# Optimization experiments

Measured on AMD Instinct MI355X. Metric: run time of the kernel, lower is better.

## Reference

```python
import jax, jax.numpy as jnp
import numpy as np

N_NODES = 16384
N_EDGES = 262144
D = 300
N_GRAPHS = 64


def setup_inputs() -> dict:
    key = jax.random.key(0)
    ks = jax.random.split(key, 16)
    s = 0.05  # small init scale for numerical stability
    inp = {
        "node_feats": jax.random.normal(ks[0], (N_NODES, D), jnp.float32),
        "W_lift": jax.random.normal(ks[1], (D, D), jnp.float32) * s,
        "b_lift": jnp.zeros((D,), jnp.float32),
        "Wf1": jax.random.normal(ks[2], (D, D), jnp.float32) * s,
        "bf1": jnp.zeros((D,), jnp.float32),
        "Wo1": jax.random.normal(ks[3], (D, D), jnp.float32) * s,
        "bo1": jnp.zeros((D,), jnp.float32),
        "Wf2": jax.random.normal(ks[4], (D, D), jnp.float32) * s,
        "bf2": jnp.zeros((D,), jnp.float32),
        "Wo2": jax.random.normal(ks[5], (D, D), jnp.float32) * s,
        "bo2": jnp.zeros((D,), jnp.float32),
        "Wf3": jax.random.normal(ks[6], (D, D), jnp.float32) * s,
        "bf3": jnp.zeros((D,), jnp.float32),
        "Wo3": jax.random.normal(ks[7], (D, D), jnp.float32) * s,
        "bo3": jnp.zeros((D,), jnp.float32),
        "W_ro": jax.random.normal(ks[8], (D, 2), jnp.float32) * s,
        "b_ro": jnp.zeros((2,), jnp.float32),
        "src": jax.random.randint(ks[9], (N_EDGES,), 0, N_NODES, jnp.int32),
        "dst": jax.random.randint(ks[10], (N_EDGES,), 0, N_NODES, jnp.int32),
        "graph_ids": jnp.sort(jax.random.randint(ks[11], (N_NODES,), 0, N_GRAPHS, jnp.int32)),
    }
    return inp


def _mp_layer(h, Wf, bf, Wo, bo, src, dst):
    # message: relu Dense on gathered src feats; reduce: segment-sum into dst nodes
    msg = jax.nn.relu(h[src] @ Wf + bf)                      # [E, D]
    agg = jax.ops.segment_sum(msg, dst, num_segments=N_NODES)  # [N, D]
    return jax.nn.relu(agg @ Wo + bo)                        # output Dense+ReLU


def reference(node_feats, W_lift, b_lift, Wf1, bf1, Wo1, bo1, Wf2, bf2, Wo2, bo2,
              Wf3, bf3, Wo3, bo3, W_ro, b_ro, src, dst, graph_ids):
    h = node_feats @ W_lift + b_lift  # lift, no activation
    h = _mp_layer(h, Wf1, bf1, Wo1, bo1, src, dst)
    h = _mp_layer(h, Wf2, bf2, Wo2, bo2, src, dst)
    h = _mp_layer(h, Wf3, bf3, Wo3, bo3, src, dst)
    probs = jax.nn.softmax(h @ W_ro + b_ro, axis=-1)         # readout Dense(softmax)
    logits = jax.ops.segment_sum(probs, graph_ids, num_segments=N_GRAPHS)  # dgl.sum_nodes
    return logits
```

## Files before the change

### kernel.cpp

```cpp
#include <hip/hip_runtime.h>
#include <hip/hip_bf16.h>

#define N_NODES 16384
#define N_EDGES 262144
#define GD 300
#define DP 320
#define N_GRAPHS 64
#define NTILE 5
#define CAP 96

typedef short bf16x8 __attribute__((ext_vector_type(8)));
typedef float f32x4 __attribute__((ext_vector_type(4)));

__device__ static inline unsigned short f2bf(float v) {
  __hip_bfloat16 b = __float2bfloat16(v);
  return __builtin_bit_cast(unsigned short, b);
}
__device__ static inline float bf2f(unsigned short u) {
  return __bfloat162float(__builtin_bit_cast(__hip_bfloat16, u));
}

#define GLOAD_LDS16(g, l)                                                    \
  __builtin_amdgcn_global_load_lds(                                          \
      (const __attribute__((address_space(1))) void*)(g),                    \
      (__attribute__((address_space(3))) void*)(l), 16, 0, 0)

constexpr int ATILE = 8192;
constexpr int AFULL = 5 * ATILE;
constexpr int BBUF = 40960;
constexpr int EPITCH = 328;
constexpr size_t WSZ = (size_t)DP * DP;
static_assert(64 * EPITCH * 2 <= AFULL + 2 * BBUF, "epilogue bounce fits");

template <bool RELU1, bool TILED, bool FUSE2, bool RO, bool CONVF>
__global__ __launch_bounds__(512, 2) void gemm_f(
    const unsigned short* __restrict__ A, const float* __restrict__ nf,
    const unsigned short* __restrict__ Wt1,
    const float* __restrict__ bias1, const unsigned short* __restrict__ Wt2,
    const float* __restrict__ bias2, unsigned short* __restrict__ C,
    const float* __restrict__ Wro, const float* __restrict__ bro,
    const int* __restrict__ gid, float* __restrict__ out) {
  __shared__ __align__(16) char smem[AFULL + 2 * BBUF];
  __shared__ float wroL[2 * DP];
  __shared__ float rowacc[2 * 64];
  __shared__ float binsL[2 * N_GRAPHS];

  const int bm = blockIdx.x * 64;
  const int t = threadIdx.x;
  const int w = t >> 6, l = t & 63;
  const int wr = w & 1;
  const int wc = w >> 1;
  const int cl = l & 15, q = l >> 4;
  const int lr = l >> 3;
  const int sg = (l & 7) ^ lr;

  if (RO) {
    for (int i = t; i < DP; i += 512) {
      wroL[2 * i] = (i < GD) ? Wro[2 * i] : 0.f;
      wroL[2 * i + 1] = (i < GD) ? Wro[2 * i + 1] : 0.f;
    }
    if (t < 128) rowacc[t] = 0.f;
    if (t < 2 * N_GRAPHS) binsL[t] = 0.f;
  }

  auto stageB = [&](const unsigned short* W, int tk, int buf) {
    char* lb = smem + AFULL + buf * BBUF;
#pragma unroll
    for (int i = 0; i < 5; ++i) {
      int c = w + 8 * i;
      GLOAD_LDS16(W + (size_t)(c * 8 + lr) * DP + tk * 64 + 8 * sg,
                  lb + c * 1024);
    }
  };

  f32x4 acc[2][5] = {};

  auto compute = [&](const char* lA, const char* lB) {
#pragma unroll
    for (int ks = 0; ks < 2; ++ks) {
      bf16x8 a[2], b[5];
#pragma unroll
      for (int m = 0; m < 2; ++m) {
        int r = wr * 32 + m * 16 + cl;
        int slot = (ks * 4 + q) ^ (r & 7);
        a[m] = *(const bf16x8*)(lA + r * 128 + slot * 16);
      }
#pragma unroll
      for (int n = 0; n < 5; ++n) {
        int r = wc * 80 + n * 16 + cl;
        int slot = (ks * 4 + q) ^ (r & 7);
        b[n] = *(const bf16x8*)(lB + r * 128 + slot * 16);
      }
#pragma unroll
      for (int m = 0; m < 2; ++m)
#pragma unroll
        for (int n = 0; n < 5; ++n)
          acc[m][n] = __builtin_amdgcn_mfma_f32_16x16x32_bf16(a[m], b[n],
                                                              acc[m][n], 0, 0, 0);
    }
  };

  stageB(Wt1, 0, 0);
  if (CONVF) {
    const int r = t >> 3;
    const int ls = t & 7;
    const float* rp = nf + (size_t)(bm + r) * GD;
#pragma unroll
    for (int p = 0; p < 5; ++p) {
      int c0 = p * 64 + ls * 8;
      bf16x8 o;
      if (c0 + 8 <= GD) {
        float4 a = *(const float4*)(rp + c0);
        float4 b = *(const float4*)(rp + c0 + 4);
        o[0] = f2bf(a.x); o[1] = f2bf(a.y); o[2] = f2bf(a.z); o[3] = f2bf(a.w);
        o[4] = f2bf(b.x); o[5] = f2bf(b.y); o[6] = f2bf(b.z); o[7] = f2bf(b.w);
      } else {
#pragma unroll
        for (int i = 0; i < 8; ++i) {
          int c = c0 + i;
          o[i] = f2bf(c < GD ? rp[c] : 0.f);
        }
      }
      *(bf16x8*)(smem + p * ATILE + r * 128 + ((ls ^ (r & 7)) << 4)) = o;
    }
    asm volatile("s_waitcnt lgkmcnt(0)" ::: "memory");
  } else {
#pragma unroll
    for (int p = 0; p < 5; ++p)
      GLOAD_LDS16(A + (size_t)(bm + w * 8 + lr) * DP + p * 64 + 8 * sg,
                  smem + p * ATILE + w * 1024);
  }

  for (int tk = 0; tk < 5; ++tk) {
    __builtin_amdgcn_s_barrier();
    if (tk + 1 < 5) {
      stageB(Wt1, tk + 1, (tk + 1) & 1);
      asm volatile("s_waitcnt vmcnt(5)" ::: "memory");
    } else if (FUSE2) {
      stageB(Wt2, 0, 1);
      asm volatile("s_waitcnt vmcnt(5)" ::: "memory");
    } else {
      asm volatile("s_waitcnt vmcnt(0)" ::: "memory");
    }
    __builtin_amdgcn_s_barrier();
    compute(smem + tk * ATILE, smem + AFULL + (tk & 1) * BBUF);
  }

  if (FUSE2) {
    __syncthreads();
#pragma unroll
    for (int n = 0; n < 5; ++n) {
      int col = wc * 80 + n * 16 + cl;
      float bv = bias1[col];
      int kt = col >> 6, kin = col & 63;
#pragma unroll
      for (int m = 0; m < 2; ++m) {
#pragma unroll
        for (int r = 0; r < 4; ++r) {
          int row = wr * 32 + m * 16 + q * 4 + r;
          float v = acc[m][n][r] + bv;
          if (RELU1) v = fmaxf(v, 0.f);
          int byte = kt * ATILE + row * 128 + (((kin >> 3) ^ (row & 7)) << 4) +
                     ((kin & 7) << 1);
          *(unsigned short*)(smem + byte) = f2bf(v);
        }
      }
    }
    asm volatile("s_waitcnt lgkmcnt(0)" ::: "memory");
#pragma unroll
    for (int m = 0; m < 2; ++m)
#pragma unroll
      for (int n = 0; n < 5; ++n) acc[m][n] = f32x4{0.f, 0.f, 0.f, 0.f};

    for (int tk = 0; tk < 5; ++tk) {
      __builtin_amdgcn_s_barrier();
      if (tk + 1 < 5) {
        stageB(Wt2, tk + 1, tk & 1);
        asm volatile("s_waitcnt vmcnt(5)" ::: "memory");
      } else {
        asm volatile("s_waitcnt vmcnt(0)" ::: "memory");
      }
      __builtin_amdgcn_s_barrier();
      compute(smem + tk * ATILE, smem + AFULL + ((tk + 1) & 1) * BBUF);
    }
  }

  if (!RO) {
    const float* bp = FUSE2 ? bias2 : bias1;
    const bool relu = FUSE2 ? true : RELU1;
    __syncthreads();
    unsigned short* ep = (unsigned short*)smem;
#pragma unroll
    for (int n = 0; n < 5; ++n) {
      int col = wc * 80 + n * 16 + cl;
      float bv = bp[col];
#pragma unroll
      for (int m = 0; m < 2; ++m) {
#pragma unroll
        for (int r = 0; r < 4; ++r) {
          int row = wr * 32 + m * 16 + q * 4 + r;
          float v = acc[m][n][r] + bv;
          if (relu) v = fmaxf(v, 0.f);
          ep[row * EPITCH + col] = f2bf(v);
        }
      }
    }
    __syncthreads();
    {
      const int row = t >> 3, c0 = (t & 7) * 40;
#pragma unroll
      for (int gch = 0; gch < 5; ++gch) {
        int col = c0 + gch * 8;
        bf16x8 v = *(const bf16x8*)(ep + row * EPITCH + col);
        size_t idx;
        if (TILED)
          idx = ((size_t)(col >> 6) * N_NODES + (bm + row)) * 64 + (col & 63);
        else
          idx = (size_t)(bm + row) * DP + col;
        *(bf16x8*)(C + idx) = v;
      }
    }
  } else {
    float bv[5];
#pragma unroll
    for (int n = 0; n < 5; ++n) bv[n] = bias1[wc * 80 + n * 16 + cl];
#pragma unroll
    for (int m = 0; m < 2; ++m) {
#pragma unroll
      for (int r = 0; r < 4; ++r) {
        float s0 = 0.f, s1 = 0.f;
#pragma unroll
        for (int n = 0; n < 5; ++n) {
          int col = wc * 80 + n * 16 + cl;
          float v = fmaxf(acc[m][n][r] + bv[n], 0.f);
          s0 += v * wroL[2 * col];
          s1 += v * wroL[2 * col + 1];
        }
#pragma unroll
        for (int off = 1; off < 16; off <<= 1) {
          s0 += __shfl_xor(s0, off);
          s1 += __shfl_xor(s1, off);
        }
        if (cl == 0) {
          int row = wr * 32 + m * 16 + q * 4 + r;
          atomicAdd(&rowacc[2 * row], s0);
          atomicAdd(&rowacc[2 * row + 1], s1);
        }
      }
    }
    __syncthreads();
    if (t < 64) {
      float d0 = rowacc[2 * t] + bro[0];
      float d1 = rowacc[2 * t + 1] + bro[1];
      float mx = fmaxf(d0, d1);
      float e0 = expf(d0 - mx), e1 = expf(d1 - mx);
      float inv = 1.f / (e0 + e1);
      int g = gid[bm + t];
      atomicAdd(&binsL[2 * g], e0 * inv);
      atomicAdd(&binsL[2 * g + 1], e1 * inv);
    }
    __syncthreads();
    if (t < 2 * N_GRAPHS) {
      float v = binsL[t];
      if (v != 0.f) atomicAdd(&out[t], v);
    }
  }
}

__global__ void scatter_pad(const int* __restrict__ src, const int* __restrict__ dst,
                            int* __restrict__ cnt, int* __restrict__ pad,
                            float* __restrict__ out, int out_n) {
  if (blockIdx.x == 0 && threadIdx.x < out_n) out[threadIdx.x] = 0.f;
  int e = blockIdx.x * blockDim.x + threadIdx.x;
  if (e >= N_EDGES) return;
  int d = dst[e];
  int pos = atomicAdd(&cnt[d], 1);
  if (pos < CAP) pad[(size_t)d * CAP + pos] = src[e];
}

__global__ __launch_bounds__(256) void spmm_tiled(
    const unsigned short* __restrict__ Mt, const int* __restrict__ cnt,
    const int* __restrict__ pad, unsigned short* __restrict__ agg) {
  const int tile = blockIdx.y;
  const int wv = threadIdx.x >> 6;
  const int l = threadIdx.x & 63;
  const int g = l >> 3;
  const int cs = l & 7;
  const int node = blockIdx.x * 32 + wv * 8 + g;
  const unsigned short* base = Mt + (size_t)tile * N_NODES * 64 + cs * 8;
  const int* lst = pad + (size_t)node * CAP;

  const int j1 = min(cnt[node], CAP);
  int j = 0;
  float acc[8] = {};
  for (; j + 16 <= j1; j += 16) {
    bf16x8 v[16];
#pragma unroll
    for (int u = 0; u < 16; ++u)
      v[u] = *(const bf16x8*)(base + (size_t)lst[j + u] * 64);
#pragma unroll
    for (int u = 0; u < 16; ++u)
#pragma unroll
      for (int i = 0; i < 8; ++i) acc[i] += bf2f(v[u][i]);
  }
  if (j + 8 <= j1) {
    bf16x8 v[8];
#pragma unroll
    for (int u = 0; u < 8; ++u)
      v[u] = *(const bf16x8*)(base + (size_t)lst[j + u] * 64);
#pragma unroll
    for (int u = 0; u < 8; ++u)
#pragma unroll
      for (int i = 0; i < 8; ++i) acc[i] += bf2f(v[u][i]);
    j += 8;
  }
  if (j + 4 <= j1) {
    bf16x8 v[4];
#pragma unroll
    for (int u = 0; u < 4; ++u)
      v[u] = *(const bf16x8*)(base + (size_t)lst[j + u] * 64);
#pragma unroll
    for (int u = 0; u < 4; ++u)
#pragma unroll
      for (int i = 0; i < 8; ++i) acc[i] += bf2f(v[u][i]);
    j += 4;
  }
  for (; j < j1; ++j) {
    bf16x8 v = *(const bf16x8*)(base + (size_t)lst[j] * 64);
#pragma unroll
    for (int i = 0; i < 8; ++i) acc[i] += bf2f(v[i]);
  }
  bf16x8 o;
#pragma unroll
  for (int i = 0; i < 8; ++i) o[i] = f2bf(acc[i]);
  *(bf16x8*)(agg + (size_t)node * DP + tile * 64 + cs * 8) = o;
}

struct WPtrs {
  const float* W[7];
  const float* b[7];
};

__global__ __launch_bounds__(256) void prep_kernel(
    WPtrs p, unsigned short* __restrict__ Wt, float* __restrict__ biasP,
    int* __restrict__ cnt) {
  __shared__ unsigned short ld[64][33];
  const int t = threadIdx.x;
  const int wb = blockIdx.x;

  if (wb < 64) cnt[wb * 256 + t] = 0;

  const int wi = wb / 50;
  const int blk = wb - wi * 50;
  const int kt = blk / 5;
  const int nt = blk - kt * 5;
  const int k0 = kt * 32, n0 = nt * 64;
  const float* W = p.W[wi];

#pragma unroll
  for (int ps = 0; ps < 8; ++ps) {
    int idx = t + 256 * ps;
    int rr = idx >> 6, cc = idx & 63;
    float v = (k0 + rr < GD && n0 + cc < GD) ? W[(size_t)(k0 + rr) * GD + n0 + cc] : 0.f;
    ld[cc][rr] = f2bf(v);
  }
  __syncthreads();
#pragma unroll
  for (int ps = 0; ps < 8; ++ps) {
    int idx = t + 256 * ps;
    int nn = idx >> 5, kk = idx & 31;
    Wt[(size_t)wi * WSZ + (size_t)(n0 + nn) * DP + k0 + kk] = ld[nn][kk];
  }
  if (blk == 0) {
    for (int i = t; i < DP; i += 256)
      biasP[(size_t)wi * DP + i] = (i < GD) ? p.b[wi][i] : 0.f;
  }
}

extern "C" void kernel_launch(void* const* d_in, const int* in_sizes, int n_in,
                              void* d_out, int out_size, void* d_ws, size_t ws_size,
                              hipStream_t stream) {
  const float* node_feats = (const float*)d_in[0];
  const float* W_ro = (const float*)d_in[15];
  const float* b_ro = (const float*)d_in[16];
  const int* src = (const int*)d_in[17];
  const int* dst = (const int*)d_in[18];
  const int* gid = (const int*)d_in[19];
  float* out = (float*)d_out;

  WPtrs wp;
  wp.W[0] = (const float*)d_in[1];   wp.b[0] = (const float*)d_in[2];
  wp.W[1] = (const float*)d_in[3];   wp.b[1] = (const float*)d_in[4];
  wp.W[2] = (const float*)d_in[5];   wp.b[2] = (const float*)d_in[6];
  wp.W[3] = (const float*)d_in[7];   wp.b[3] = (const float*)d_in[8];
  wp.W[4] = (const float*)d_in[9];   wp.b[4] = (const float*)d_in[10];
  wp.W[5] = (const float*)d_in[11];  wp.b[5] = (const float*)d_in[12];
  wp.W[6] = (const float*)d_in[13];  wp.b[6] = (const float*)d_in[14];

  char* p = (char*)d_ws;
  unsigned short* X = (unsigned short*)p;  p += (size_t)N_NODES * DP * 2;
  unsigned short* Y = (unsigned short*)p;  p += (size_t)N_NODES * DP * 2;
  unsigned short* Wt = (unsigned short*)p; p += (size_t)7 * WSZ * 2;
  float* biasP = (float*)p;                p += 7 * DP * 4;
  int* cnt = (int*)p;                      p += N_NODES * 4;
  int* pad = (int*)p;                      p += (size_t)N_NODES * CAP * 4;

  prep_kernel<<<350, 256, 0, stream>>>(wp, Wt, biasP, cnt);
  scatter_pad<<<N_EDGES / 256, 256, 0, stream>>>(src, dst, cnt, pad, out, out_size);

  dim3 sgrid(N_NODES / 32, NTILE);

  gemm_f<false, true, true, false, true><<<256, 512, 0, stream>>>(
      nullptr, node_feats, Wt + 0 * WSZ, biasP + 0 * DP,
      Wt + 1 * WSZ, biasP + 1 * DP, Y, nullptr, nullptr, nullptr, nullptr);
  spmm_tiled<<<sgrid, 256, 0, stream>>>(Y, cnt, pad, X);
  gemm_f<true, true, true, false, false><<<256, 512, 0, stream>>>(
      X, nullptr, Wt + 2 * WSZ, biasP + 2 * DP,
      Wt + 3 * WSZ, biasP + 3 * DP, Y, nullptr, nullptr, nullptr, nullptr);
  spmm_tiled<<<sgrid, 256, 0, stream>>>(Y, cnt, pad, X);
  gemm_f<true, true, true, false, false><<<256, 512, 0, stream>>>(
      X, nullptr, Wt + 4 * WSZ, biasP + 4 * DP,
      Wt + 5 * WSZ, biasP + 5 * DP, Y, nullptr, nullptr, nullptr, nullptr);
  spmm_tiled<<<sgrid, 256, 0, stream>>>(Y, cnt, pad, X);
  gemm_f<true, false, false, true, false><<<256, 512, 0, stream>>>(
      X, nullptr, Wt + 6 * WSZ, biasP + 6 * DP, nullptr, nullptr, nullptr,
      W_ro, b_ro, gid, out);
}
```

Before: 155.1 us.

## Triple-buffer weight tiles and merge fused GEMM loops into one pipelined loop

```diff
diff --git a/kernel.cpp b/kernel.cpp
--- a/kernel.cpp
+++ b/kernel.cpp
@@ -30,7 +30,8 @@
 constexpr int BBUF = 40960;
 constexpr int EPITCH = 328;
 constexpr size_t WSZ = (size_t)DP * DP;
-static_assert(64 * EPITCH * 2 <= AFULL + 2 * BBUF, "epilogue bounce fits");
+static_assert(AFULL + 3 * BBUF == 163840, "exactly 160 KiB");
+static_assert(64 * EPITCH * 2 <= AFULL + 3 * BBUF, "epilogue bounce fits");
 
 template <bool RELU1, bool TILED, bool FUSE2, bool RO, bool CONVF>
 __global__ __launch_bounds__(512, 2) void gemm_f(
@@ -40,10 +41,7 @@
     const float* __restrict__ bias2, unsigned short* __restrict__ C,
     const float* __restrict__ Wro, const float* __restrict__ bro,
     const int* __restrict__ gid, float* __restrict__ out) {
-  __shared__ __align__(16) char smem[AFULL + 2 * BBUF];
-  __shared__ float wroL[2 * DP];
-  __shared__ float rowacc[2 * 64];
-  __shared__ float binsL[2 * N_GRAPHS];
+  __shared__ __align__(16) char smem[AFULL + 3 * BBUF];
 
   const int bm = blockIdx.x * 64;
   const int t = threadIdx.x;
@@ -54,21 +52,18 @@
   const int lr = l >> 3;
   const int sg = (l & 7) ^ lr;
 
-  if (RO) {
-    for (int i = t; i < DP; i += 512) {
-      wroL[2 * i] = (i < GD) ? Wro[2 * i] : 0.f;
-      wroL[2 * i + 1] = (i < GD) ? Wro[2 * i + 1] : 0.f;
-    }
-    if (t < 128) rowacc[t] = 0.f;
-    if (t < 2 * N_GRAPHS) binsL[t] = 0.f;
-  }
-
-  auto stageB = [&](const unsigned short* W, int tk, int buf) {
+  float b1r[5];
+  if (FUSE2) {
+#pragma unroll
+    for (int n = 0; n < 5; ++n) b1r[n] = bias1[wc * 80 + n * 16 + cl];
+  }
+
+  auto stageB = [&](const unsigned short* W, int kt, int buf) {
     char* lb = smem + AFULL + buf * BBUF;
 #pragma unroll
     for (int i = 0; i < 5; ++i) {
       int c = w + 8 * i;
-      GLOAD_LDS16(W + (size_t)(c * 8 + lr) * DP + tk * 64 + 8 * sg,
+      GLOAD_LDS16(W + (size_t)(c * 8 + lr) * DP + kt * 64 + 8 * sg,
                   lb + c * 1024);
     }
   };
@@ -100,7 +95,6 @@
     }
   };
 
-  stageB(Wt1, 0, 0);
   if (CONVF) {
     const int r = t >> 3;
     const int ls = t & 7;
@@ -130,59 +124,48 @@
       GLOAD_LDS16(A + (size_t)(bm + w * 8 + lr) * DP + p * 64 + 8 * sg,
                   smem + p * ATILE + w * 1024);
   }
-
-  for (int tk = 0; tk < 5; ++tk) {
+  stageB(Wt1, 0, 0);
+  stageB(Wt1, 1, 1);
+
+  constexpr int NT = FUSE2 ? 10 : 5;
+  for (int i = 0; i < NT; ++i) {
+    if (FUSE2 && i == 5) {
+      __builtin_amdgcn_s_barrier();
+#pragma unroll
+      for (int n = 0; n < 5; ++n) {
+        int col = wc * 80 + n * 16 + cl;
+        int kt = col >> 6, kin = col & 63;
+#pragma unroll
+        for (int m = 0; m < 2; ++m) {
+#pragma unroll
+          for (int r = 0; r < 4; ++r) {
+            int row = wr * 32 + m * 16 + q * 4 + r;
+            float v = acc[m][n][r] + b1r[n];
+            if (RELU1) v = fmaxf(v, 0.f);
+            int byte = kt * ATILE + row * 128 +
+                       (((kin >> 3) ^ (row & 7)) << 4) + ((kin & 7) << 1);
+            *(unsigned short*)(smem + byte) = f2bf(v);
+          }
+        }
+      }
+      asm volatile("s_waitcnt lgkmcnt(0)" ::: "memory");
+#pragma unroll
+      for (int m = 0; m < 2; ++m)
+#pragma unroll
+        for (int n = 0; n < 5; ++n) acc[m][n] = f32x4{0.f, 0.f, 0.f, 0.f};
+    }
     __builtin_amdgcn_s_barrier();
-    if (tk + 1 < 5) {
-      stageB(Wt1, tk + 1, (tk + 1) & 1);
-      asm volatile("s_waitcnt vmcnt(5)" ::: "memory");
-    } else if (FUSE2) {
-      stageB(Wt2, 0, 1);
+    if (i + 2 < NT) {
+      const unsigned short* W = (FUSE2 && i + 2 >= 5) ? Wt2 : Wt1;
+      stageB(W, (i + 2) % 5, (i + 2) % 3);
+      asm volatile("s_waitcnt vmcnt(10)" ::: "memory");
+    } else if (i + 1 < NT) {
       asm volatile("s_waitcnt vmcnt(5)" ::: "memory");
     } else {
       asm volatile("s_waitcnt vmcnt(0)" ::: "memory");
     }
     __builtin_amdgcn_s_barrier();
-    compute(smem + tk * ATILE, smem + AFULL + (tk & 1) * BBUF);
-  }
-
-  if (FUSE2) {
-    __syncthreads();
-#pragma unroll
-    for (int n = 0; n < 5; ++n) {
-      int col = wc * 80 + n * 16 + cl;
-      float bv = bias1[col];
-      int kt = col >> 6, kin = col & 63;
-#pragma unroll
-      for (int m = 0; m < 2; ++m) {
-#pragma unroll
-        for (int r = 0; r < 4; ++r) {
-          int row = wr * 32 + m * 16 + q * 4 + r;
-          float v = acc[m][n][r] + bv;
-          if (RELU1) v = fmaxf(v, 0.f);
-          int byte = kt * ATILE + row * 128 + (((kin >> 3) ^ (row & 7)) << 4) +
-                     ((kin & 7) << 1);
-          *(unsigned short*)(smem + byte) = f2bf(v);
-        }
-      }
-    }
-    asm volatile("s_waitcnt lgkmcnt(0)" ::: "memory");
-#pragma unroll
-    for (int m = 0; m < 2; ++m)
-#pragma unroll
-      for (int n = 0; n < 5; ++n) acc[m][n] = f32x4{0.f, 0.f, 0.f, 0.f};
-
-    for (int tk = 0; tk < 5; ++tk) {
-      __builtin_amdgcn_s_barrier();
-      if (tk + 1 < 5) {
-        stageB(Wt2, tk + 1, tk & 1);
-        asm volatile("s_waitcnt vmcnt(5)" ::: "memory");
-      } else {
-        asm volatile("s_waitcnt vmcnt(0)" ::: "memory");
-      }
-      __builtin_amdgcn_s_barrier();
-      compute(smem + tk * ATILE, smem + AFULL + ((tk + 1) & 1) * BBUF);
-    }
+    compute(smem + (i % 5) * ATILE, smem + AFULL + (i % 3) * BBUF);
   }
 
   if (!RO) {
@@ -221,6 +204,18 @@
       }
     }
   } else {
+    __syncthreads();
+    float* wroL = (float*)smem;
+    float* rowacc = wroL + 2 * DP;
+    float* binsL = rowacc + 128;
+    for (int i = t; i < DP; i += 512) {
+      wroL[2 * i] = (i < GD) ? Wro[2 * i] : 0.f;
+      wroL[2 * i + 1] = (i < GD) ? Wro[2 * i + 1] : 0.f;
+    }
+    if (t < 128) rowacc[t] = 0.f;
+    if (t >= 128 && t < 256) binsL[t - 128] = 0.f;
+    __syncthreads();
+
     float bv[5];
 #pragma unroll
     for (int n = 0; n < 5; ++n) bv[n] = bias1[wc * 80 + n * 16 + cl];
```

Result: no change. 158.1 us (+1.9%).
